# Performance work log

Measured on AMD Instinct MI355X. Metric: run time of the kernel, lower is better.

## Reference

```python
import jax, jax.numpy as jnp
import numpy as np

H, DM, LQ, LK, DK, DV = 16, 1024, 2048, 2048, 64, 64
B = 2

def setup_inputs() -> dict:
    key = jax.random.key(0)
    ks = jax.random.split(key, 12)
    s = 0.02  # init scale for weights
    return {
        "Q": jax.random.normal(ks[0], (B, LQ, DM), jnp.float32),
        "K": jax.random.normal(ks[1], (B, LK, DM), jnp.float32),
        "V": jax.random.normal(ks[2], (B, LK, DM), jnp.float32),
        "mask": jax.random.randint(ks[3], (B, LQ), 0, 2, jnp.int32),
        "W_Q": jax.random.normal(ks[4], (H * DK, DM), jnp.float32) * s,
        "b_Q": jnp.zeros((H * DK,), jnp.float32),
        "W_K": jax.random.normal(ks[5], (H * DK, DM), jnp.float32) * s,
        "b_K": jnp.zeros((H * DK,), jnp.float32),
        "W_V": jax.random.normal(ks[6], (H * DV, DM), jnp.float32) * s,
        "b_V": jnp.zeros((H * DV,), jnp.float32),
        "W_O": jax.random.normal(ks[7], (DM, H * DV), jnp.float32) * s,
        "b_O": jnp.zeros((DM,), jnp.float32),
    }

def reference(Q, K, V, mask, W_Q, b_Q, W_K, b_K, W_V, b_V, W_O, b_O):
    b = Q.shape[0]
    q = (Q @ W_Q.T + b_Q).reshape(b, LQ, H, DK)
    k = (K @ W_K.T + b_K).reshape(b, LK, H, DK)
    v = (V @ W_V.T + b_V).reshape(b, LK, H, DV)
    # scores: [b, h, q, k]
    A = jnp.einsum('bqhd,bkhd->bhqk', q, k) / jnp.sqrt(jnp.float32(DK))
    # mask masks whole QUERY rows; softmax is over the query axis (dim=1 in torch's [B*h, lq, lk])
    A = jnp.where(mask[:, None, :, None] == 0, -jnp.inf, A)
    alpha = jax.nn.softmax(A, axis=2)  # over query axis, per original masked branch
    out = jnp.einsum('bhqk,bkhd->bqhd', alpha, v).reshape(b, LQ, H * DV)
    return out @ W_O.T + b_O + Q  # output proj + residual
```

## Files before the change

kernel.cpp:

```cpp
#include <hip/hip_runtime.h>
#include <hip/hip_bf16.h>
#include <stdint.h>

using frag8 = __attribute__((ext_vector_type(8))) short;
using f32x4 = __attribute__((ext_vector_type(4))) float;

#define MFMA16 __builtin_amdgcn_mfma_f32_16x16x32_bf16

#if __has_builtin(__builtin_amdgcn_exp2f)
#define EXP2F(x) __builtin_amdgcn_exp2f(x)
#else
#define EXP2F(x) __expf((x) * 0.6931471805599453f)
#endif
#if __has_builtin(__builtin_amdgcn_rcpf)
#define RCPF(x) __builtin_amdgcn_rcpf(x)
#else
#define RCPF(x) (1.0f / (x))
#endif

#define SCALE_Q 0.18033688011112042f

__device__ __forceinline__ short f2bf(float f) {
    union { float f; uint32_t u; } x; x.f = f;
    uint32_t r = x.u + 0x7fffu + ((x.u >> 16) & 1u);
    return (short)(r >> 16);
}
__device__ __forceinline__ float bf2f(short s) {
    union { uint32_t u; float f; } x; x.u = ((uint32_t)(uint16_t)s) << 16;
    return x.f;
}
__device__ __forceinline__ uint32_t pack2bf(float a, float b) {
    float2 t; t.x = a; t.y = b;
    __hip_bfloat162 h = __float22bfloat162_rn(t);
    union { __hip_bfloat162 h; uint32_t u; } c; c.h = h;
    return c.u;
}
__device__ __forceinline__ frag8 cvt8(float4 a, float4 b) {
    frag8 r;
    r[0] = f2bf(a.x); r[1] = f2bf(a.y); r[2] = f2bf(a.z); r[3] = f2bf(a.w);
    r[4] = f2bf(b.x); r[5] = f2bf(b.y); r[6] = f2bf(b.z); r[7] = f2bf(b.w);
    return r;
}
__device__ __forceinline__ frag8 addbf8(uint4 x, uint4 y) {
    frag8 r;
    const ushort* xs = (const ushort*)&x;
    const ushort* ys = (const ushort*)&y;
#pragma unroll
    for (int i = 0; i < 8; i++)
        r[i] = f2bf(bf2f((short)xs[i]) + bf2f((short)ys[i]));
    return r;
}

__global__ __launch_bounds__(64) void k_compact(const int* __restrict__ mask,
                                                int* __restrict__ idx,
                                                int* __restrict__ nU) {
    const int b = blockIdx.x, ln = threadIdx.x;
    const int* m = mask + b * 2048;
    int* id = idx + b * 2048;
    int base = 0;
    for (int c = 0; c < 32; c++) {
        int i = c * 64 + ln;
        int mv = m[i];
        unsigned long long bal = __ballot(mv != 0);
        int rank = __popcll(bal & ((1ull << ln) - 1ull));
        if (mv) id[base + rank] = i;
        base += __popcll(bal);
    }
    if (ln == 0) nU[b] = base;
    int nUr = (base + 63) & ~63;
    for (int i = base + ln; i < nUr; i += 64) id[i] = 0;
}

__global__ __launch_bounds__(256) void k_zero2(uint4* __restrict__ a,
                                               uint4* __restrict__ b, int n16) {
    int i = blockIdx.x * 256 + threadIdx.x;
    if (i < n16) { uint4 z = {0, 0, 0, 0}; a[i] = z; b[i] = z; }
}

__global__ __launch_bounds__(256) void k_psum(short* __restrict__ p0,
                                              const short* __restrict__ p1, int n8) {
    int i = blockIdx.x * 256 + threadIdx.x;
    int st = gridDim.x * 256;
    for (; i < n8; i += st) {
        uint4 a = ((const uint4*)p0)[i];
        uint4 b = ((const uint4*)p1)[i];
        frag8 r = addbf8(a, b);
        ((uint4*)p0)[i] = *(uint4*)&r;
    }
}

__global__ __launch_bounds__(256) void k_gather(const short* __restrict__ q_s,
                                                const int* __restrict__ idx,
                                                const int* __restrict__ nU,
                                                short* __restrict__ q_c) {
    const int bh = blockIdx.x, tile = blockIdx.y, b = bh >> 4;
    const int n = nU[b], nUr = (n + 63) & ~63;
    const int i = tile * 64 + (threadIdx.x >> 2);
    if (i >= nUr) return;
    const int src = idx[b * 2048 + i];
    const uint4* sp = (const uint4*)(q_s + ((size_t)bh * 2048 + src) * 64);
    uint4* dp = (uint4*)(q_c + ((size_t)bh * 2048 + i) * 64);
    const int c = threadIdx.x & 3;
    dp[c] = sp[c];
    dp[c + 4] = sp[c + 4];
}

__global__ __launch_bounds__(256) void k_cvt_w(
    const float* __restrict__ s0, const float* __restrict__ s1,
    const float* __restrict__ s2, const float* __restrict__ s3,
    short* __restrict__ d0, short* __restrict__ d1,
    short* __restrict__ d2, short* __restrict__ d3) {
    const int W4 = 262144;
    int i = blockIdx.x * 256 + threadIdx.x;
    int st = gridDim.x * 256;
    for (; i < 4 * W4; i += st) {
        int seg = i / W4, j = i - seg * W4;
        const float* sp = seg == 0 ? s0 : seg == 1 ? s1 : seg == 2 ? s2 : s3;
        short* dp = seg == 0 ? d0 : seg == 1 ? d1 : seg == 2 ? d2 : d3;
        float4 v = ((const float4*)sp)[j];
        ushort4 o;
        o.x = (uint16_t)f2bf(v.x); o.y = (uint16_t)f2bf(v.y);
        o.z = (uint16_t)f2bf(v.z); o.w = (uint16_t)f2bf(v.w);
        ((ushort4*)dp)[j] = o;
    }
}

__device__ __forceinline__ void stage64x128(const short* __restrict__ g, int rs,
                                            short* lds, int tid) {
#pragma unroll
    for (int j = 0; j < 2; j++) {
        int chunk = j * 256 + tid;
        int row = chunk >> 3, c = chunk & 7;
        int sc = c ^ (row & 7);
        __builtin_amdgcn_global_load_lds(
            (const __attribute__((address_space(1))) uint32_t*)(g + (size_t)row * rs + sc * 8),
            (__attribute__((address_space(3))) uint32_t*)(lds + (j * 256 + (tid & 192)) * 8),
            16, 0, 0);
    }
}
__device__ __forceinline__ frag8 ldswz(const short* lds, int row, int cc) {
    return *(const frag8*)(lds + row * 64 + ((cc ^ (row & 7)) << 3));
}

__device__ __forceinline__ void stage_tiles(const short* __restrict__ As,
                                            const short* __restrict__ Bs,
                                            short* lA, short* lB,
                                            int w, int ln) {
#pragma unroll
    for (int j = 0; j < 2; j++) {
        int cb = (w * 2 + j) * 64;
        int c  = cb + ln;
        int row = c >> 2, c8 = c & 3;
        __builtin_amdgcn_global_load_lds(
            (const __attribute__((address_space(1))) uint32_t*)(As + row * 1024 + c8 * 8),
            (__attribute__((address_space(3))) uint32_t*)(lA + cb * 8), 16, 0, 0);
        __builtin_amdgcn_global_load_lds(
            (const __attribute__((address_space(1))) uint32_t*)(Bs + row * 1024 + c8 * 8),
            (__attribute__((address_space(3))) uint32_t*)(lB + cb * 8), 16, 0, 0);
    }
}
__device__ __forceinline__ void stage_b(const short* __restrict__ Bs,
                                        short* lB, int w, int ln) {
#pragma unroll
    for (int j = 0; j < 2; j++) {
        int cb = (w * 2 + j) * 64;
        int c  = cb + ln;
        int row = c >> 2, c8 = c & 3;
        __builtin_amdgcn_global_load_lds(
            (const __attribute__((address_space(1))) uint32_t*)(Bs + row * 1024 + c8 * 8),
            (__attribute__((address_space(3))) uint32_t*)(lB + cb * 8), 16, 0, 0);
    }
}

__global__ __launch_bounds__(256) void k_proj3(
    const float* __restrict__ A0, const float* __restrict__ A1, const float* __restrict__ A2,
    const short* __restrict__ B0, const short* __restrict__ B1, const short* __restrict__ B2,
    const float* __restrict__ bias0, const float* __restrict__ bias1, const float* __restrict__ bias2,
    short* __restrict__ dst0, short* __restrict__ dst1, short* __restrict__ dst2) {
    __shared__ short lA[2][4096];
    __shared__ short lB[2][4096];
    const int z = blockIdx.z;
    const float* A  = z == 0 ? A0 : z == 1 ? A1 : A2;
    const short* Bt = z == 0 ? B0 : z == 1 ? B1 : B2;
    const float* bias = z == 0 ? bias0 : z == 1 ? bias1 : bias2;
    short* dst = z == 0 ? dst0 : z == 1 ? dst1 : dst2;
    const float scale = z == 0 ? SCALE_Q : 1.0f;

    const int tid = threadIdx.x, w = tid >> 6, ln = tid & 63;
    const int wm = w >> 1, wn = w & 1, r16 = ln & 15, g = ln >> 4;
    const int tn = blockIdx.x * 128, tm = blockIdx.y * 128;
    const float* Ab = A + (size_t)tm * 1024;
    const short* Bb = Bt + (size_t)tn * 1024;

    const int cb0 = (w * 2 + 0) * 64 + ln, cb1 = (w * 2 + 1) * 64 + ln;
    const int rA0 = cb0 >> 2, cA0 = cb0 & 3, rA1 = cb1 >> 2, cA1 = cb1 & 3;

    float4 ra[4];
    f32x4 acc[4][4] = {};

    {
        const float* a0 = Ab + (size_t)rA0 * 1024 + cA0 * 8;
        ra[0] = *(const float4*)a0; ra[1] = *(const float4*)(a0 + 4);
        const float* a1 = Ab + (size_t)rA1 * 1024 + cA1 * 8;
        ra[2] = *(const float4*)a1; ra[3] = *(const float4*)(a1 + 4);
    }
    stage_b(Bb, &lB[0][0], w, ln);
    *(frag8*)&lA[0][cb0 * 8] = cvt8(ra[0], ra[1]);
    *(frag8*)&lA[0][cb1 * 8] = cvt8(ra[2], ra[3]);

    int buf = 0;
    for (int ks = 0; ks < 32; ks++) {
        if (ks + 1 < 32) {
            const float* a0 = Ab + (size_t)rA0 * 1024 + (ks + 1) * 32 + cA0 * 8;
            ra[0] = *(const float4*)a0; ra[1] = *(const float4*)(a0 + 4);
            const float* a1 = Ab + (size_t)rA1 * 1024 + (ks + 1) * 32 + cA1 * 8;
            ra[2] = *(const float4*)a1; ra[3] = *(const float4*)(a1 + 4);
        }
        __syncthreads();
        if (ks + 1 < 32)
            stage_b(Bb + (ks + 1) * 32, &lB[buf ^ 1][0], w, ln);
        frag8 af[4], bg[4];
#pragma unroll
        for (int mf = 0; mf < 4; mf++)
            af[mf] = *(const frag8*)&lA[buf][(wm * 64 + mf * 16 + r16) * 32 + g * 8];
#pragma unroll
        for (int nf = 0; nf < 4; nf++)
            bg[nf] = *(const frag8*)&lB[buf][(wn * 64 + nf * 16 + r16) * 32 + g * 8];
#pragma unroll
        for (int mf = 0; mf < 4; mf++)
#pragma unroll
            for (int nf = 0; nf < 4; nf++)
                acc[mf][nf] = MFMA16(af[mf], bg[nf], acc[mf][nf], 0, 0, 0);
        if (ks + 1 < 32) {
            *(frag8*)&lA[buf ^ 1][cb0 * 8] = cvt8(ra[0], ra[1]);
            *(frag8*)&lA[buf ^ 1][cb1 * 8] = cvt8(ra[2], ra[3]);
        }
        buf ^= 1;
    }
#pragma unroll
    for (int mf = 0; mf < 4; mf++)
#pragma unroll
        for (int nf = 0; nf < 4; nf++)
#pragma unroll
            for (int r = 0; r < 4; r++) {
                int m = tm + wm * 64 + mf * 16 + g * 4 + r;
                int n = tn + wn * 64 + nf * 16 + r16;
                float val = (acc[mf][nf][r] + bias[n]) * scale;
                int b = m >> 11, seq = m & 2047, h = n >> 6, d = n & 63;
                dst[((size_t)(b * 16 + h) * 2048 + seq) * 64 + d] = f2bf(val);
            }
}

__global__ __launch_bounds__(256, 4) void k_stats(const short* __restrict__ k_s,
                                                  const short* __restrict__ q_c,
                                                  const int* __restrict__ nU,
                                                  const short* __restrict__ v_s,
                                                  short* __restrict__ vhatT) {
    __shared__ short lQ[2][4096];
    __shared__ float lD[64];
    __shared__ short lT[64 * 70];
    const int wg = blockIdx.x;
    const int lin = (wg & 7) * 128 + (wg >> 3);
    const int bh = lin >> 5, kt = lin & 31;
    const int b = bh >> 4;
    const int n = nU[b], nUr = (n + 63) & ~63;
    const int tid = threadIdx.x, w = tid >> 6, ln = tid & 63;
    const int r16 = ln & 15, g = ln >> 4;
    const int kbase = kt * 64 + w * 16;

    const short* kp = k_s + ((size_t)bh * 2048 + kbase) * 64;
    frag8 kf[2];
#pragma unroll
    for (int kk = 0; kk < 2; kk++)
        kf[kk] = *(const frag8*)(kp + r16 * 64 + kk * 32 + g * 8);

    const short* qsp = q_c + (size_t)bh * 2048 * 64;
    float dacc[4] = {};
    const f32x4 z4 = {0.f, 0.f, 0.f, 0.f};

    if (nUr > 0) {
        stage64x128(qsp, 64, &lQ[0][0], tid);
        int buf = 0;
        for (int qb = 0; qb < nUr; qb += 64) {
            __syncthreads();
            if (qb + 64 < nUr)
                stage64x128(qsp + (size_t)(qb + 64) * 64, 64, &lQ[buf ^ 1][0], tid);
            const short* Qc = &lQ[buf][0];
#pragma unroll
            for (int nf = 0; nf < 4; nf++) {
                float fm = (qb + nf * 16 + r16 < n) ? 1.0f : 0.0f;
                frag8 bq0 = ldswz(Qc, nf * 16 + r16, g);
                frag8 bq1 = ldswz(Qc, nf * 16 + r16, 4 + g);
                f32x4 s = MFMA16(kf[0], bq0, z4, 0, 0, 0);
                s = MFMA16(kf[1], bq1, s, 0, 0, 0);
#pragma unroll
                for (int r = 0; r < 4; r++)
                    dacc[r] += fm * EXP2F(s[r]);
            }
            buf ^= 1;
        }
    }
#pragma unroll
    for (int r = 0; r < 4; r++) {
        float v = dacc[r];
#pragma unroll
        for (int off = 1; off < 16; off <<= 1)
            v += __shfl_xor(v, off, 16);
        dacc[r] = v;
    }
    if (r16 == 0) {
#pragma unroll
        for (int r = 0; r < 4; r++)
            lD[w * 16 + g * 4 + r] = RCPF(dacc[r]);
    }
    const short* vrow = v_s + ((size_t)bh * 2048 + kt * 64) * 64;
#pragma unroll
    for (int i = 0; i < 4; i++) {
        int idx4 = i * 256 + tid;
        int row = idx4 >> 4, c4 = idx4 & 15;
        uint2 u = *(const uint2*)(vrow + (size_t)row * 64 + c4 * 4);
        *(uint32_t*)&lT[row * 70 + c4 * 4]     = u.x;
        *(uint32_t*)&lT[row * 70 + c4 * 4 + 2] = u.y;
    }
    __syncthreads();
    {
        int d = tid >> 2, kc = tid & 3;
        short* dstp = vhatT + ((size_t)bh * 64 + d) * 2048 + kt * 64 + kc * 16;
        uint32_t wd[8];
#pragma unroll
        for (int j2 = 0; j2 < 8; j2++) {
            int k0 = kc * 16 + j2 * 2;
            float v0 = bf2f(lT[k0 * 70 + d]) * lD[k0];
            float v1 = bf2f(lT[(k0 + 1) * 70 + d]) * lD[k0 + 1];
            wd[j2] = pack2bf(v0, v1);
        }
        uint4 o0 = {wd[0], wd[1], wd[2], wd[3]};
        uint4 o1 = {wd[4], wd[5], wd[6], wd[7]};
        *(uint4*)dstp = o0;
        *((uint4*)dstp + 1) = o1;
    }
}

__global__ __launch_bounds__(256, 4) void k_apply(const short* __restrict__ q_c,
                                                  const short* __restrict__ k_s,
                                                  const short* __restrict__ vhatT,
                                                  const int* __restrict__ idx,
                                                  const int* __restrict__ nU,
                                                  short* __restrict__ p0,
                                                  short* __restrict__ p1) {
    __shared__ short lK[2][4096];
    __shared__ short lV[2][4096];
    __shared__ short lP[64 * 64];
    const int wg = blockIdx.x;
    const int lin = (wg & 7) * 256 + (wg >> 3);
    const int bh = lin >> 6, rem = lin & 63, qt = rem >> 1, sp = rem & 1;
    const int b = bh >> 4, h = bh & 15;
    const int n = nU[b];
    if (qt * 64 >= n) return;
    const int tid = threadIdx.x, w = tid >> 6, ln = tid & 63;
    const int r16 = ln & 15, g = ln >> 4;

    const short* qp = q_c + ((size_t)bh * 2048 + qt * 64 + w * 16) * 64;
    frag8 qf[2];
#pragma unroll
    for (int kk = 0; kk < 2; kk++)
        qf[kk] = *(const frag8*)(qp + r16 * 64 + kk * 32 + g * 8);

    const short* kp = k_s + ((size_t)bh * 2048 + sp * 1024) * 64;
    const short* vp = vhatT + (size_t)bh * 64 * 2048 + sp * 1024;

    f32x4 oacc[4] = {};
    const f32x4 z4 = {0.f, 0.f, 0.f, 0.f};
    const int prow = w * 16 + r16, rx = prow & 7;

    stage64x128(kp, 64, &lK[0][0], tid);
    stage64x128(vp, 2048, &lV[0][0], tid);
    int buf = 0;
    for (int kb = 0; kb < 1024; kb += 64) {
        __syncthreads();
        if (kb + 64 < 1024) {
            stage64x128(kp + (size_t)(kb + 64) * 64, 64, &lK[buf ^ 1][0], tid);
            stage64x128(vp + kb + 64, 2048, &lV[buf ^ 1][0], tid);
        }
        const short* Kc = &lK[buf][0];
        const short* Vc = &lV[buf][0];
        frag8 vb[4][2];
#pragma unroll
        for (int nf = 0; nf < 4; nf++)
#pragma unroll
            for (int kk = 0; kk < 2; kk++)
                vb[nf][kk] = ldswz(Vc, nf * 16 + r16, kk * 4 + g);
#pragma unroll
        for (int mf2 = 0; mf2 < 4; mf2++) {
            f32x4 s = z4;
#pragma unroll
            for (int kk = 0; kk < 2; kk++)
                s = MFMA16(ldswz(Kc, mf2 * 16 + r16, kk * 4 + g), qf[kk], s, 0, 0, 0);
            float e0 = EXP2F(s[0]), e1 = EXP2F(s[1]);
            float e2 = EXP2F(s[2]), e3 = EXP2F(s[3]);
            uint2 pk;
            pk.x = pack2bf(e0, e1);
            pk.y = pack2bf(e2, e3);
            int o = mf2 * 32 + g * 8;
            int addr = prow * 128 + (((o >> 4) ^ rx) << 4) + (o & 15);
            *(uint2*)((char*)lP + addr) = pk;
        }
        frag8 pa[2];
#pragma unroll
        for (int kk = 0; kk < 2; kk++)
            pa[kk] = *(const frag8*)((char*)lP + prow * 128 + (((kk * 4 + g) ^ rx) << 4));
#pragma unroll
        for (int nf = 0; nf < 4; nf++)
#pragma unroll
            for (int kk = 0; kk < 2; kk++)
                oacc[nf] = MFMA16(pa[kk], vb[nf][kk], oacc[nf], 0, 0, 0);
        buf ^= 1;
    }
    short* op = sp ? p1 : p0;
#pragma unroll
    for (int r = 0; r < 4; r++) {
        int lq = qt * 64 + w * 16 + g * 4 + r;
        if (lq < n) {
            int qg = idx[b * 2048 + lq];
#pragma unroll
            for (int nf = 0; nf < 4; nf++) {
                int d = nf * 16 + r16;
                op[((size_t)(b * 2048 + qg)) * 1024 + h * 64 + d] = f2bf(oacc[nf][r]);
            }
        }
    }
}

__global__ __launch_bounds__(256) void k_final(const short* __restrict__ A,
                                               const short* __restrict__ Bt,
                                               const float* __restrict__ bias,
                                               const float* __restrict__ Qres,
                                               float* __restrict__ out) {
    __shared__ short lA[2][4096];
    __shared__ short lB[2][4096];
    const int tid = threadIdx.x, w = tid >> 6, ln = tid & 63;
    const int wm = w >> 1, wn = w & 1, r16 = ln & 15, g = ln >> 4;
    const int tn = blockIdx.x * 128, tm = blockIdx.y * 128;
    const short* Ab = A + (size_t)tm * 1024;
    const short* Bb = Bt + (size_t)tn * 1024;

    f32x4 acc[4][4] = {};
    stage_tiles(Ab, Bb, &lA[0][0], &lB[0][0], w, ln);
    int buf = 0;
    for (int ks = 0; ks < 32; ks++) {
        __syncthreads();
        if (ks + 1 < 32)
            stage_tiles(Ab + (ks + 1) * 32, Bb + (ks + 1) * 32,
                        &lA[buf ^ 1][0], &lB[buf ^ 1][0], w, ln);
        frag8 af[4], bg[4];
#pragma unroll
        for (int mf = 0; mf < 4; mf++)
            af[mf] = *(const frag8*)&lA[buf][(wm * 64 + mf * 16 + r16) * 32 + g * 8];
#pragma unroll
        for (int nf = 0; nf < 4; nf++)
            bg[nf] = *(const frag8*)&lB[buf][(wn * 64 + nf * 16 + r16) * 32 + g * 8];
#pragma unroll
        for (int mf = 0; mf < 4; mf++)
#pragma unroll
            for (int nf = 0; nf < 4; nf++)
                acc[mf][nf] = MFMA16(af[mf], bg[nf], acc[mf][nf], 0, 0, 0);
        buf ^= 1;
    }
#pragma unroll
    for (int mf = 0; mf < 4; mf++)
#pragma unroll
        for (int nf = 0; nf < 4; nf++)
#pragma unroll
            for (int r = 0; r < 4; r++) {
                int m = tm + wm * 64 + mf * 16 + g * 4 + r;
                int n = tn + wn * 64 + nf * 16 + r16;
                float val = acc[mf][nf][r] + bias[n] + Qres[(size_t)m * 1024 + n];
                out[(size_t)m * 1024 + n] = val;
            }
}

extern "C" void kernel_launch(void* const* d_in, const int* in_sizes, int n_in,
                              void* d_out, int out_size, void* d_ws, size_t ws_size,
                              hipStream_t stream) {
    (void)in_sizes; (void)n_in; (void)out_size; (void)ws_size;
    const float* Qf  = (const float*)d_in[0];
    const float* Kf  = (const float*)d_in[1];
    const float* Vf  = (const float*)d_in[2];
    const int*   msk = (const int*)d_in[3];
    const float* WQ  = (const float*)d_in[4];
    const float* bQ  = (const float*)d_in[5];
    const float* WK  = (const float*)d_in[6];
    const float* bK  = (const float*)d_in[7];
    const float* WV  = (const float*)d_in[8];
    const float* bV  = (const float*)d_in[9];
    const float* WO  = (const float*)d_in[10];
    const float* bO  = (const float*)d_in[11];
    float* out = (float*)d_out;

    char* p = (char*)d_ws;
    const size_t SZ_ACT = (size_t)4096 * 1024 * 2;
    const size_t SZ_W   = (size_t)1024 * 1024 * 2;
    short* q_s   = (short*)p; p += SZ_ACT;
    short* k_s   = (short*)p; p += SZ_ACT;
    short* v_s   = (short*)p; p += SZ_ACT;
    short* vhatT = (short*)p; p += SZ_ACT;
    short* p0    = (short*)p; p += SZ_ACT;
    short* q_c   = (short*)p; p += SZ_ACT;
    short* Wqb = (short*)p; p += SZ_W;
    short* Wkb = (short*)p; p += SZ_W;
    short* Wvb = (short*)p; p += SZ_W;
    short* Wob = (short*)p; p += SZ_W;
    int* idx = (int*)p; p += (size_t)2 * 2048 * 4;
    int* nU  = (int*)p; p += 256;
    short* p1 = v_s;

    k_compact<<<2, 64, 0, stream>>>(msk, idx, nU);

    k_cvt_w<<<1024, 256, 0, stream>>>(WQ, WK, WV, WO, Wqb, Wkb, Wvb, Wob);

    k_proj3<<<dim3(8, 32, 3), 256, 0, stream>>>(Qf, Kf, Vf, Wqb, Wkb, Wvb,
                                                bQ, bK, bV, q_s, k_s, v_s);

    k_gather<<<dim3(32, 32), 256, 0, stream>>>(q_s, idx, nU, q_c);

    k_stats<<<1024, 256, 0, stream>>>(k_s, q_c, nU, v_s, vhatT);

    k_zero2<<<2048, 256, 0, stream>>>((uint4*)p0, (uint4*)p1, 524288);

    k_apply<<<2048, 256, 0, stream>>>(q_c, k_s, vhatT, idx, nU, p0, p1);

    k_psum<<<2048, 256, 0, stream>>>(p0, p1, 524288);

    k_final<<<dim3(8, 32), 256, 0, stream>>>(p0, Wob, bO, Qf, out);
}
```

Baseline: 182.8 us.

## Double per-block tile height in stats/apply and remap GEMM block indices

k_stats and k_apply now give each wave 32 rows instead of 16, so each block covers 128 keys or queries. Every staged Q/K/V tile in LDS is reused across twice as many MFMAs, and the grid shrinks by half. The projection and final GEMMs switch to a 1D grid with an XCD-aware swizzle, grouping blocks that share A/B tiles so their loads hit the same L2. The trade-off is higher register and LDS use per block (launch bounds relaxed to 3) and fewer blocks, which means coarser early-exit granularity for masked query tiles.

```diff
diff --git a/kernel.cpp b/kernel.cpp
--- a/kernel.cpp
+++ b/kernel.cpp
@@ -179,7 +179,10 @@
     short* __restrict__ dst0, short* __restrict__ dst1, short* __restrict__ dst2) {
     __shared__ short lA[2][4096];
     __shared__ short lB[2][4096];
-    const int z = blockIdx.z;
+    const int wg = blockIdx.x;
+    const int tmlow = wg & 7, tnb = (wg >> 3) & 7, rest = wg >> 6;
+    const int tmh = rest & 3, z = rest >> 2;
+    const int tmb = tmlow | (tmh << 3);
     const float* A  = z == 0 ? A0 : z == 1 ? A1 : A2;
     const short* Bt = z == 0 ? B0 : z == 1 ? B1 : B2;
     const float* bias = z == 0 ? bias0 : z == 1 ? bias1 : bias2;
@@ -188,7 +191,7 @@
 
     const int tid = threadIdx.x, w = tid >> 6, ln = tid & 63;
     const int wm = w >> 1, wn = w & 1, r16 = ln & 15, g = ln >> 4;
-    const int tn = blockIdx.x * 128, tm = blockIdx.y * 128;
+    const int tn = tnb * 128, tm = tmb * 128;
     const float* Ab = A + (size_t)tm * 1024;
     const short* Bb = Bt + (size_t)tn * 1024;
 
@@ -251,31 +254,34 @@
             }
 }
 
-__global__ __launch_bounds__(256, 4) void k_stats(const short* __restrict__ k_s,
+__global__ __launch_bounds__(256, 3) void k_stats(const short* __restrict__ k_s,
                                                   const short* __restrict__ q_c,
                                                   const int* __restrict__ nU,
                                                   const short* __restrict__ v_s,
                                                   short* __restrict__ vhatT) {
     __shared__ short lQ[2][4096];
-    __shared__ float lD[64];
-    __shared__ short lT[64 * 70];
+    __shared__ float lD[128];
+    __shared__ short lT[128 * 70];
     const int wg = blockIdx.x;
-    const int lin = (wg & 7) * 128 + (wg >> 3);
-    const int bh = lin >> 5, kt = lin & 31;
+    const int x = wg & 7, r2 = wg >> 3;
+    const int kt = r2 & 15;
+    const int bh = x + 8 * (r2 >> 4);
     const int b = bh >> 4;
     const int n = nU[b], nUr = (n + 63) & ~63;
     const int tid = threadIdx.x, w = tid >> 6, ln = tid & 63;
     const int r16 = ln & 15, g = ln >> 4;
-    const int kbase = kt * 64 + w * 16;
+    const int kbase = kt * 128 + w * 32;
 
     const short* kp = k_s + ((size_t)bh * 2048 + kbase) * 64;
-    frag8 kf[2];
-#pragma unroll
-    for (int kk = 0; kk < 2; kk++)
-        kf[kk] = *(const frag8*)(kp + r16 * 64 + kk * 32 + g * 8);
+    frag8 kf[2][2];
+#pragma unroll
+    for (int mfk = 0; mfk < 2; mfk++)
+#pragma unroll
+        for (int kk = 0; kk < 2; kk++)
+            kf[mfk][kk] = *(const frag8*)(kp + (mfk * 16 + r16) * 64 + kk * 32 + g * 8);
 
     const short* qsp = q_c + (size_t)bh * 2048 * 64;
-    float dacc[4] = {};
+    float dacc[2][4] = {};
     const f32x4 z4 = {0.f, 0.f, 0.f, 0.f};
 
     if (nUr > 0) {
@@ -291,31 +297,38 @@
                 float fm = (qb + nf * 16 + r16 < n) ? 1.0f : 0.0f;
                 frag8 bq0 = ldswz(Qc, nf * 16 + r16, g);
                 frag8 bq1 = ldswz(Qc, nf * 16 + r16, 4 + g);
-                f32x4 s = MFMA16(kf[0], bq0, z4, 0, 0, 0);
-                s = MFMA16(kf[1], bq1, s, 0, 0, 0);
-#pragma unroll
-                for (int r = 0; r < 4; r++)
-                    dacc[r] += fm * EXP2F(s[r]);
+#pragma unroll
+                for (int mfk = 0; mfk < 2; mfk++) {
+                    f32x4 s = MFMA16(kf[mfk][0], bq0, z4, 0, 0, 0);
+                    s = MFMA16(kf[mfk][1], bq1, s, 0, 0, 0);
+#pragma unroll
+                    for (int r = 0; r < 4; r++)
+                        dacc[mfk][r] += fm * EXP2F(s[r]);
+                }
             }
             buf ^= 1;
         }
     }
 #pragma unroll
-    for (int r = 0; r < 4; r++) {
-        float v = dacc[r];
-#pragma unroll
-        for (int off = 1; off < 16; off <<= 1)
-            v += __shfl_xor(v, off, 16);
-        dacc[r] = v;
-    }
+    for (int mfk = 0; mfk < 2; mfk++)
+#pragma unroll
+        for (int r = 0; r < 4; r++) {
+            float v = dacc[mfk][r];
+#pragma unroll
+            for (int off = 1; off < 16; off <<= 1)
+                v += __shfl_xor(v, off, 16);
+            dacc[mfk][r] = v;
+        }
     if (r16 == 0) {
 #pragma unroll
-        for (int r = 0; r < 4; r++)
-            lD[w * 16 + g * 4 + r] = RCPF(dacc[r]);
-    }
-    const short* vrow = v_s + ((size_t)bh * 2048 + kt * 64) * 64;
-#pragma unroll
-    for (int i = 0; i < 4; i++) {
+        for (int mfk = 0; mfk < 2; mfk++)
+#pragma unroll
+            for (int r = 0; r < 4; r++)
+                lD[w * 32 + mfk * 16 + g * 4 + r] = RCPF(dacc[mfk][r]);
+    }
+    const short* vrow = v_s + ((size_t)bh * 2048 + kt * 128) * 64;
+#pragma unroll
+    for (int i = 0; i < 8; i++) {
         int idx4 = i * 256 + tid;
         int row = idx4 >> 4, c4 = idx4 & 15;
         uint2 u = *(const uint2*)(vrow + (size_t)row * 64 + c4 * 4);
@@ -325,23 +338,24 @@
     __syncthreads();
     {
         int d = tid >> 2, kc = tid & 3;
-        short* dstp = vhatT + ((size_t)bh * 64 + d) * 2048 + kt * 64 + kc * 16;
-        uint32_t wd[8];
-#pragma unroll
-        for (int j2 = 0; j2 < 8; j2++) {
-            int k0 = kc * 16 + j2 * 2;
+        short* dstp = vhatT + ((size_t)bh * 64 + d) * 2048 + kt * 128 + kc * 32;
+        uint32_t wd[16];
+#pragma unroll
+        for (int j2 = 0; j2 < 16; j2++) {
+            int k0 = kc * 32 + j2 * 2;
             float v0 = bf2f(lT[k0 * 70 + d]) * lD[k0];
             float v1 = bf2f(lT[(k0 + 1) * 70 + d]) * lD[k0 + 1];
             wd[j2] = pack2bf(v0, v1);
         }
-        uint4 o0 = {wd[0], wd[1], wd[2], wd[3]};
-        uint4 o1 = {wd[4], wd[5], wd[6], wd[7]};
-        *(uint4*)dstp = o0;
-        *((uint4*)dstp + 1) = o1;
-    }
-}
-
-__global__ __launch_bounds__(256, 4) void k_apply(const short* __restrict__ q_c,
+#pragma unroll
+        for (int j4 = 0; j4 < 4; j4++) {
+            uint4 o = {wd[j4 * 4], wd[j4 * 4 + 1], wd[j4 * 4 + 2], wd[j4 * 4 + 3]};
+            *((uint4*)dstp + j4) = o;
+        }
+    }
+}
+
+__global__ __launch_bounds__(256, 3) void k_apply(const short* __restrict__ q_c,
                                                   const short* __restrict__ k_s,
                                                   const short* __restrict__ vhatT,
                                                   const int* __restrict__ idx,
@@ -350,28 +364,31 @@
                                                   short* __restrict__ p1) {
     __shared__ short lK[2][4096];
     __shared__ short lV[2][4096];
-    __shared__ short lP[64 * 64];
+    __shared__ short lP[128 * 64];
     const int wg = blockIdx.x;
-    const int lin = (wg & 7) * 256 + (wg >> 3);
-    const int bh = lin >> 6, rem = lin & 63, qt = rem >> 1, sp = rem & 1;
+    const int x = wg & 7, r2 = wg >> 3;
+    const int qt = r2 & 15, y = r2 >> 4;
+    const int bhsp = (y << 3) | x;
+    const int bh = bhsp >> 1, sp = bhsp & 1;
     const int b = bh >> 4, h = bh & 15;
     const int n = nU[b];
-    if (qt * 64 >= n) return;
+    if (qt * 128 >= n) return;
     const int tid = threadIdx.x, w = tid >> 6, ln = tid & 63;
     const int r16 = ln & 15, g = ln >> 4;
 
-    const short* qp = q_c + ((size_t)bh * 2048 + qt * 64 + w * 16) * 64;
-    frag8 qf[2];
-#pragma unroll
-    for (int kk = 0; kk < 2; kk++)
-        qf[kk] = *(const frag8*)(qp + r16 * 64 + kk * 32 + g * 8);
+    const short* qp = q_c + ((size_t)bh * 2048 + qt * 128 + w * 32) * 64;
+    frag8 qf[2][2];
+#pragma unroll
+    for (int qi = 0; qi < 2; qi++)
+#pragma unroll
+        for (int kk = 0; kk < 2; kk++)
+            qf[qi][kk] = *(const frag8*)(qp + (qi * 16 + r16) * 64 + kk * 32 + g * 8);
 
     const short* kp = k_s + ((size_t)bh * 2048 + sp * 1024) * 64;
     const short* vp = vhatT + (size_t)bh * 64 * 2048 + sp * 1024;
 
-    f32x4 oacc[4] = {};
+    f32x4 oacc[2][4] = {};
     const f32x4 z4 = {0.f, 0.f, 0.f, 0.f};
-    const int prow = w * 16 + r16, rx = prow & 7;
 
     stage64x128(kp, 64, &lK[0][0], tid);
     stage64x128(vp, 2048, &lV[0][0], tid);
@@ -391,44 +408,56 @@
             for (int kk = 0; kk < 2; kk++)
                 vb[nf][kk] = ldswz(Vc, nf * 16 + r16, kk * 4 + g);
 #pragma unroll
-        for (int mf2 = 0; mf2 < 4; mf2++) {
-            f32x4 s = z4;
+        for (int qi = 0; qi < 2; qi++) {
+            const int prow = w * 32 + qi * 16 + r16;
+            const int rx = prow & 7;
+#pragma unroll
+            for (int mf2 = 0; mf2 < 4; mf2++) {
+                f32x4 s = z4;
+#pragma unroll
+                for (int kk = 0; kk < 2; kk++)
+                    s = MFMA16(ldswz(Kc, mf2 * 16 + r16, kk * 4 + g), qf[qi][kk], s, 0, 0, 0);
+                float e0 = EXP2F(s[0]), e1 = EXP2F(s[1]);
+                float e2 = EXP2F(s[2]), e3 = EXP2F(s[3]);
+                uint2 pk;
+                pk.x = pack2bf(e0, e1);
+                pk.y = pack2bf(e2, e3);
+                int o = mf2 * 32 + g * 8;
+                int addr = prow * 128 + (((o >> 4) ^ rx) << 4) + (o & 15);
+                *(uint2*)((char*)lP + addr) = pk;
+            }
+        }
+#pragma unroll
+        for (int qi = 0; qi < 2; qi++) {
+            const int prow = w * 32 + qi * 16 + r16;
+            const int rx = prow & 7;
+            frag8 pa[2];
 #pragma unroll
             for (int kk = 0; kk < 2; kk++)
-                s = MFMA16(ldswz(Kc, mf2 * 16 + r16, kk * 4 + g), qf[kk], s, 0, 0, 0);
-            float e0 = EXP2F(s[0]), e1 = EXP2F(s[1]);
-            float e2 = EXP2F(s[2]), e3 = EXP2F(s[3]);
-            uint2 pk;
-            pk.x = pack2bf(e0, e1);
-            pk.y = pack2bf(e2, e3);
-            int o = mf2 * 32 + g * 8;
-            int addr = prow * 128 + (((o >> 4) ^ rx) << 4) + (o & 15);
-            *(uint2*)((char*)lP + addr) = pk;
-        }
-        frag8 pa[2];
-#pragma unroll
-        for (int kk = 0; kk < 2; kk++)
-            pa[kk] = *(const frag8*)((char*)lP + prow * 128 + (((kk * 4 + g) ^ rx) << 4));
-#pragma unroll
-        for (int nf = 0; nf < 4; nf++)
-#pragma unroll
-            for (int kk = 0; kk < 2; kk++)
-                oacc[nf] = MFMA16(pa[kk], vb[nf][kk], oacc[nf], 0, 0, 0);
+                pa[kk] = *(const frag8*)((char*)lP + prow * 128 + (((kk * 4 + g) ^ rx) << 4));
+#pragma unroll
+            for (int nf = 0; nf < 4; nf++)
+#pragma unroll
+                for (int kk = 0; kk < 2; kk++)
+                    oacc[qi][nf] = MFMA16(pa[kk], vb[nf][kk], oacc[qi][nf], 0, 0, 0);
+        }
         buf ^= 1;
     }
     short* op = sp ? p1 : p0;
 #pragma unroll
-    for (int r = 0; r < 4; r++) {
-        int lq = qt * 64 + w * 16 + g * 4 + r;
-        if (lq < n) {
-            int qg = idx[b * 2048 + lq];
-#pragma unroll
-            for (int nf = 0; nf < 4; nf++) {
-                int d = nf * 16 + r16;
-                op[((size_t)(b * 2048 + qg)) * 1024 + h * 64 + d] = f2bf(oacc[nf][r]);
+    for (int qi = 0; qi < 2; qi++)
+#pragma unroll
+        for (int r = 0; r < 4; r++) {
+            int lq = qt * 128 + w * 32 + qi * 16 + g * 4 + r;
+            if (lq < n) {
+                int qg = idx[b * 2048 + lq];
+#pragma unroll
+                for (int nf = 0; nf < 4; nf++) {
+                    int d = nf * 16 + r16;
+                    op[((size_t)(b * 2048 + qg)) * 1024 + h * 64 + d] = f2bf(oacc[qi][nf][r]);
+                }
             }
         }
-    }
 }
 
 __global__ __launch_bounds__(256) void k_final(const short* __restrict__ A,
@@ -438,9 +467,12 @@
                                                float* __restrict__ out) {
     __shared__ short lA[2][4096];
     __shared__ short lB[2][4096];
+    const int wg = blockIdx.x;
+    const int tmb = (wg & 7) | ((wg >> 6) << 3);
+    const int tnb = (wg >> 3) & 7;
     const int tid = threadIdx.x, w = tid >> 6, ln = tid & 63;
     const int wm = w >> 1, wn = w & 1, r16 = ln & 15, g = ln >> 4;
-    const int tn = blockIdx.x * 128, tm = blockIdx.y * 128;
+    const int tn = tnb * 128, tm = tmb * 128;
     const short* Ab = A + (size_t)tm * 1024;
     const short* Bb = Bt + (size_t)tn * 1024;
 
@@ -518,18 +550,18 @@
 
     k_cvt_w<<<1024, 256, 0, stream>>>(WQ, WK, WV, WO, Wqb, Wkb, Wvb, Wob);
 
-    k_proj3<<<dim3(8, 32, 3), 256, 0, stream>>>(Qf, Kf, Vf, Wqb, Wkb, Wvb,
-                                                bQ, bK, bV, q_s, k_s, v_s);
+    k_proj3<<<768, 256, 0, stream>>>(Qf, Kf, Vf, Wqb, Wkb, Wvb,
+                                     bQ, bK, bV, q_s, k_s, v_s);
 
     k_gather<<<dim3(32, 32), 256, 0, stream>>>(q_s, idx, nU, q_c);
 
-    k_stats<<<1024, 256, 0, stream>>>(k_s, q_c, nU, v_s, vhatT);
+    k_stats<<<512, 256, 0, stream>>>(k_s, q_c, nU, v_s, vhatT);
 
     k_zero2<<<2048, 256, 0, stream>>>((uint4*)p0, (uint4*)p1, 524288);
 
-    k_apply<<<2048, 256, 0, stream>>>(q_c, k_s, vhatT, idx, nU, p0, p1);
+    k_apply<<<1024, 256, 0, stream>>>(q_c, k_s, vhatT, idx, nU, p0, p1);
 
     k_psum<<<2048, 256, 0, stream>>>(p0, p1, 524288);
 
-    k_final<<<dim3(8, 32), 256, 0, stream>>>(p0, Wob, bO, Qf, out);
-}
+    k_final<<<256, 256, 0, stream>>>(p0, Wob, bO, Qf, out);
+}
```

Result: faster. 161.5 us (-11.7%).
